# Performance work log

Hardware: AMD Instinct MI355X
Metric: run time of the kernel (lower is better)

The kernel has to match this reference:

```python
import jax, jax.numpy as jnp
from jax import lax
import numpy as np

DN = ('NCHW', 'OIHW', 'NCHW')


def conv(x, w, b, pad=0):
    y = lax.conv_general_dilated(x, w, (1, 1), [(pad, pad), (pad, pad)],
                                 dimension_numbers=DN)
    return y + b[None, :, None, None]


def deconv(x, w, b, stride=1):
    # PyTorch ConvTranspose2d weight is (in, out, kH, kW); equivalent conv uses
    # flipped, in/out-transposed kernel with lhs dilation = stride, pad = k-1.
    k = w.shape[2]
    wt = jnp.flip(w, (2, 3)).transpose(1, 0, 2, 3)
    y = lax.conv_general_dilated(x, wt, (1, 1), [(k - 1, k - 1), (k - 1, k - 1)],
                                 lhs_dilation=(stride, stride), dimension_numbers=DN)
    return y + b[None, :, None, None]


def maxpool2(x):
    return lax.reduce_window(x, -jnp.inf, lax.max, (1, 1, 2, 2), (1, 1, 2, 2), 'VALID')


def setup_inputs() -> dict:
    key = jax.random.key(0)
    ks = jax.random.split(key, 12)
    B = 256

    def he(k, shape, fan_in):
        return jax.random.normal(k, shape, jnp.float32) * np.sqrt(2.0 / fan_in)

    inp = {
        'x': jax.random.normal(ks[0], (B, 1, 28, 28), jnp.float32),
        # encoder convs
        'w1': he(ks[1], (128, 1, 5, 5), 1 * 25), 'b1': jnp.zeros((128,), jnp.float32),
        'w2': he(ks[2], (128, 128, 5, 5), 128 * 25), 'b2': jnp.zeros((128,), jnp.float32),
        'w3': he(ks[3], (128, 128, 5, 5), 128 * 25), 'b3': jnp.zeros((128,), jnp.float32),
        # decoder transposed convs (torch shape: in, out, kH, kW)
        't1w': he(ks[4], (128, 128, 4, 4), 128 * 16), 't1b': jnp.zeros((128,), jnp.float32),
        't2w': he(ks[5], (128, 128, 4, 4), 128 * 16), 't2b': jnp.zeros((128,), jnp.float32),
        't3w': he(ks[6], (128, 128, 5, 5), 128 * 25), 't3b': jnp.zeros((128,), jnp.float32),
        't4w': he(ks[7], (128, 128, 5, 5), 128 * 25), 't4b': jnp.zeros((128,), jnp.float32),
        # mu_net 1x1 conv
        'mw': he(ks[8], (1, 128, 1, 1), 128), 'mb': jnp.zeros((1,), jnp.float32),
        # codebook: Embedding(128, 128), init ~ N(0, 1)
        'dict_w': jax.random.normal(ks[9], (128, 128), jnp.float32),
    }
    return inp


def reference(x, w1, b1, w2, b2, w3, b3,
              t1w, t1b, t2w, t2b, t3w, t3b, t4w, t4b,
              mw, mb, dict_w):
    BETA, RATE = 0.25, 5.0
    # ---- encoder ----
    h = jax.nn.relu(conv(x, w1, b1, pad=0))          # (B,128,24,24)
    h = jax.nn.relu(conv(h, w2, b2, pad=2))          # (B,128,24,24)
    h = maxpool2(h)                                  # (B,128,12,12)
    h = conv(h, w3, b3, pad=2)                       # (B,128,12,12)
    z = maxpool2(h)                                  # (B,128,6,6)

    # ---- nearest_neighbor (faithful: argmax of distance, as in the source) ----
    z_sg = lax.stop_gradient(z)
    z2 = jnp.sum(z_sg * z_sg, axis=1, keepdims=True)          # (B,1,6,6)
    w2n = jnp.sum(dict_w * dict_w, axis=1)                     # (K,)
    cross = jnp.einsum('bchw,kc->bkhw', z_sg, lax.stop_gradient(dict_w))
    d2 = z2 + w2n[None, :, None, None] - 2.0 * cross           # (B,K,6,6)
    index = jnp.argmax(d2, axis=1)                             # (B,6,6) int

    # ---- embedding gather ----
    val = dict_w[index].transpose(0, 3, 1, 2)                  # (B,128,6,6)

    # ---- decoder on detached codes ----
    f = lax.stop_gradient(val)
    f = jax.nn.relu(deconv(f, t1w, t1b, stride=1))             # (B,128,9,9)
    f = jax.nn.relu(deconv(f, t2w, t2b, stride=2))             # (B,128,20,20)
    f = jax.nn.relu(deconv(f, t3w, t3b, stride=1))             # (B,128,24,24)
    f = jax.nn.relu(deconv(f, t4w, t4b, stride=1))             # (B,128,28,28)
    mu = conv(f, mw, mb, pad=0)                                # (B,1,28,28)

    loss_rec = jnp.mean((mu - x) ** 2)
    dict_loss = jnp.mean((val - lax.stop_gradient(z)) ** 2) * RATE
    enc_loss = jnp.mean((z - lax.stop_gradient(val)) ** 2) * BETA * RATE
    var_loss = jnp.zeros((), jnp.float32)
    losses = jnp.stack([loss_rec, dict_loss, enc_loss, var_loss])
    return losses, index
```

## Files before the change

kernel.cpp:

```cpp
#include <hip/hip_runtime.h>
#include <hip/hip_bf16.h>


#define B_ 256

typedef __attribute__((ext_vector_type(8))) short s16x8;
typedef __attribute__((ext_vector_type(4))) short s16x4;
typedef __attribute__((ext_vector_type(8))) _Float16 f16x8;
typedef __attribute__((ext_vector_type(4))) float f32x4;

__device__ inline ushort f2bf(float f) {
  union { __hip_bfloat16 h; ushort u; } cv;
  cv.h = __float2bfloat16(f);
  return cv.u;
}

__global__ __launch_bounds__(256) void prep_all(
    const float* __restrict__ t1w, const float* __restrict__ t3w,
    const float* __restrict__ t4w, const float* __restrict__ t2w,
    const float* __restrict__ w2, const float* __restrict__ w3,
    ushort* __restrict__ wp1, ushort* __restrict__ wp3,
    ushort* __restrict__ wp4, ushort* __restrict__ wp2,
    _Float16* __restrict__ w2h, _Float16* __restrict__ w2l,
    _Float16* __restrict__ w3h, _Float16* __restrict__ w3l) {
  const int b = blockIdx.x, t = threadIdx.x;
  if (b < 1024) {
    int idx = b * 256 + t;
    int ci = idx & 127, co = (idx >> 7) & 127, tap = idx >> 14;
    wp1[idx] = f2bf(t1w[((size_t)ci * 128 + co) * 16 + (15 - tap)]);
  } else if (b < 2624) {
    int idx = (b - 1024) * 256 + t;
    int ci = idx & 127, co = (idx >> 7) & 127, tap = idx >> 14;
    wp3[idx] = f2bf(t3w[((size_t)ci * 128 + co) * 25 + (24 - tap)]);
  } else if (b < 4224) {
    int idx = (b - 2624) * 256 + t;
    int ci = idx & 127, co = (idx >> 7) & 127, tap = idx >> 14;
    wp4[idx] = f2bf(t4w[((size_t)ci * 128 + co) * 25 + (24 - tap)]);
  } else if (b < 5248) {
    int idx = (b - 4224) * 256 + t;
    int ci = idx & 127, co = (idx >> 7) & 127;
    int tap = (idx >> 14) & 3, pp = idx >> 16;
    int u = tap >> 1, v = tap & 1, py = pp >> 1, px = pp & 1;
    wp2[idx] = f2bf(
        t2w[(((size_t)ci * 128 + co) * 4 + (py + 2 * u)) * 4 + (px + 2 * v)]);
  } else if (b < 6848) {
    int idx = (b - 5248) * 256 + t;
    int ci = idx & 127, co = (idx >> 7) & 127, tap = idx >> 14;
    float v = w2[((size_t)co * 128 + ci) * 25 + tap];
    _Float16 h = (_Float16)v;
    w2h[idx] = h;
    w2l[idx] = (_Float16)(v - (float)h);
  } else {
    int idx = (b - 6848) * 256 + t;
    int ci = idx & 127, co = (idx >> 7) & 127, tap = idx >> 14;
    float v = w3[((size_t)co * 128 + ci) * 25 + tap];
    _Float16 h = (_Float16)v;
    w3h[idx] = h;
    w3l[idx] = (_Float16)(v - (float)h);
  }
}

__global__ __launch_bounds__(256) void conv1_kernel(
    const float* __restrict__ x, const float* __restrict__ w,
    const float* __restrict__ b, _Float16* __restrict__ oh,
    _Float16* __restrict__ ol) {
  const int n = blockIdx.x;
  __shared__ float xl[784];
  __shared__ float wl[128 * 25];
  __shared__ float bl[128];
  const int t = threadIdx.x;
  for (int e = t; e < 784; e += 256) xl[e] = x[n * 784 + e];
  for (int e = t; e < 3200; e += 256) wl[e] = w[e];
  if (t < 128) bl[t] = b[t];
  __syncthreads();
  const size_t nb = (size_t)n * 73728;
  for (int idx = t; idx < 73728; idx += 256) {
    int co = idx & 127, p = idx >> 7;
    int y = p / 24, xx = p % 24;
    float acc = bl[co];
    const float* wc = &wl[co * 25];
#pragma unroll
    for (int ky = 0; ky < 5; ky++)
#pragma unroll
      for (int kx = 0; kx < 5; kx++)
        acc += xl[(y + ky) * 28 + xx + kx] * wc[ky * 5 + kx];
    float v = fmaxf(acc, 0.f);
    _Float16 h = (_Float16)v;
    oh[nb + idx] = h;
    ol[nb + idx] = (_Float16)(v - (float)h);
  }
}

template <int IW, int K, int PAD, int TR, bool RELU, bool OUT_F32, int PWX>
__global__ __launch_bounds__(256, 3) void conv_mfma_pool(
    const _Float16* __restrict__ inh, const _Float16* __restrict__ inl,
    const _Float16* __restrict__ wph, const _Float16* __restrict__ wpl,
    const float* __restrict__ bias, _Float16* __restrict__ outh,
    _Float16* __restrict__ outl, float* __restrict__ outf) {
  constexpr int IH = IW, OW = IW, OH = IW;
  constexpr int PW = PWX;
  constexpr int SROWS = TR + K - 1;
  constexpr int S = SROWS * PW;
  constexpr int NPOS = TR * OW;
  constexpr int NCH = NPOS / 16;
  constexpr int SCRP = NPOS + 1;
  constexpr int K2 = K * K;
  constexpr int PITCH = 40;
  constexpr int LIN_ELT = S * PITCH;
  constexpr int LIN_BYTES = 2 * LIN_ELT * 2;
  constexpr int SCR_BYTES = 64 * SCRP * 4;
  constexpr int SMEM_BYTES = LIN_BYTES > SCR_BYTES ? LIN_BYTES : SCR_BYTES;
  static_assert(NPOS % 16 == 0, "");
  static_assert(TR % 2 == 0 && OW % 2 == 0, "");
  static_assert(PW >= OW + K - 1, "");
  __shared__ __align__(16) char smem[SMEM_BYTES];
  _Float16* linh = (_Float16*)smem;
  _Float16* linl = linh + LIN_ELT;
  const int n = blockIdx.x;
  const int r0 = blockIdx.y * TR;
  const int t = threadIdx.x;
  const int wv = t >> 6;
  const int lane = t & 63;
  const int nn = lane & 15;
  const int q = lane >> 4;
  f32x4 acc0[NCH], acc1[NCH];
  int boff[NCH];
#pragma unroll
  for (int c = 0; c < NCH; c++) {
    acc0[c] = f32x4{0.f, 0.f, 0.f, 0.f};
    acc1[c] = f32x4{0.f, 0.f, 0.f, 0.f};
    int p = c * 16 + nn;
    boff[c] = ((p / OW) * PW + (p % OW)) * PITCH + q * 8;
  }
  const int rowA = wv * 16 + nn;
  const int rowB = (wv + 4) * 16 + nn;
  for (int cb = 0; cb < 4; cb++) {
    const int ci0 = cb * 32;
    __syncthreads();
    for (int e = t; e < S * 4; e += 256) {
      int sp = e >> 2, j = e & 3;
      int r = sp / PW, c = sp - r * PW;
      int ir = r0 + r - PAD, ic = c - PAD;
      f16x8 vh = {0, 0, 0, 0, 0, 0, 0, 0};
      f16x8 vl = {0, 0, 0, 0, 0, 0, 0, 0};
      if (ir >= 0 && ir < IH && ic >= 0 && ic < IW) {
        size_t g = ((size_t)n * (IH * IW) + ir * IW + ic) * 128 + ci0 + j * 8;
        vh = *(const f16x8*)&inh[g];
        vl = *(const f16x8*)&inl[g];
      }
      int st = sp * PITCH + j * 8;
      *(f16x8*)&linh[st] = vh;
      *(f16x8*)&linl[st] = vl;
    }
    __syncthreads();
    const size_t gA = (size_t)rowA * 128 + ci0 + q * 8;
    const size_t gB = (size_t)rowB * 128 + ci0 + q * 8;
    f16x8 cah0 = *(const f16x8*)&wph[gA];
    f16x8 cal0 = *(const f16x8*)&wpl[gA];
    f16x8 cah1 = *(const f16x8*)&wph[gB];
    f16x8 cal1 = *(const f16x8*)&wpl[gB];
    for (int tap = 0; tap < K2; tap++) {
      f16x8 nah0 = cah0, nal0 = cal0, nah1 = cah1, nal1 = cal1;
      if (tap + 1 < K2) {
        size_t oA = gA + (size_t)(tap + 1) * 16384;
        size_t oB = gB + (size_t)(tap + 1) * 16384;
        nah0 = *(const f16x8*)&wph[oA];
        nal0 = *(const f16x8*)&wpl[oA];
        nah1 = *(const f16x8*)&wph[oB];
        nal1 = *(const f16x8*)&wpl[oB];
      }
      const int ky = tap / K, kx = tap - ky * K;
      const int tp = (ky * PW + kx) * PITCH;
#pragma unroll
      for (int c = 0; c < NCH; c++) {
        int off = boff[c] + tp;
        f16x8 bh = *(const f16x8*)&linh[off];
        f16x8 bl = *(const f16x8*)&linl[off];
        acc0[c] =
            __builtin_amdgcn_mfma_f32_16x16x32_f16(cah0, bh, acc0[c], 0, 0, 0);
        acc0[c] =
            __builtin_amdgcn_mfma_f32_16x16x32_f16(cah0, bl, acc0[c], 0, 0, 0);
        acc0[c] =
            __builtin_amdgcn_mfma_f32_16x16x32_f16(cal0, bh, acc0[c], 0, 0, 0);
        acc1[c] =
            __builtin_amdgcn_mfma_f32_16x16x32_f16(cah1, bh, acc1[c], 0, 0, 0);
        acc1[c] =
            __builtin_amdgcn_mfma_f32_16x16x32_f16(cah1, bl, acc1[c], 0, 0, 0);
        acc1[c] =
            __builtin_amdgcn_mfma_f32_16x16x32_f16(cal1, bh, acc1[c], 0, 0, 0);
      }
      cah0 = nah0; cal0 = nal0; cah1 = nah1; cal1 = nal1;
    }
  }
  __syncthreads();
  float* scr = (float*)smem + wv * 16 * SCRP;
#pragma unroll
  for (int j = 0; j < 2; j++) {
    const int cot = (j ? wv + 4 : wv) * 16;
#pragma unroll
    for (int c = 0; c < NCH; c++) {
      f32x4 a = j ? acc1[c] : acc0[c];
#pragma unroll
      for (int r = 0; r < 4; r++) {
        float v = a[r] + bias[cot + q * 4 + r];
        if (RELU) v = fmaxf(v, 0.f);
        scr[(q * 4 + r) * SCRP + c * 16 + nn] = v;
      }
    }
    __syncthreads();
    for (int e = lane; e < 16 * (TR / 2) * (OW / 2); e += 64) {
      int co_l = e & 15;
      int rem = e >> 4;
      int pr = rem / (OW / 2), pc = rem - pr * (OW / 2);
      const float* s = scr + co_l * SCRP;
      int lp = (2 * pr) * OW + 2 * pc;
      float m =
          fmaxf(fmaxf(s[lp], s[lp + 1]), fmaxf(s[lp + OW], s[lp + OW + 1]));
      int sp_out = (r0 / 2 + pr) * (OW / 2) + pc;
      size_t go =
          ((size_t)n * ((OH / 2) * (OW / 2)) + sp_out) * 128 + cot + co_l;
      if (OUT_F32) {
        outf[go] = m;
      } else {
        _Float16 h = (_Float16)m;
        outh[go] = h;
        outl[go] = (_Float16)(m - (float)h);
      }
    }
    __syncthreads();
  }
}

__global__ __launch_bounds__(256) void vq_kernel(
    const float* __restrict__ z, const float* __restrict__ dict,
    float* __restrict__ val, ushort* __restrict__ val_bf,
    float* __restrict__ out_idx, float* __restrict__ out) {
  const int n = blockIdx.x;
  __shared__ float zl[36 * 128];
  __shared__ float d2[36 * 129];
  __shared__ float w2n[128];
  __shared__ int bk[36];
  __shared__ float red[256];
  const int t = threadIdx.x;
  const float* zn = z + (size_t)n * 4608;
  for (int e = t; e < 4608; e += 256) zl[e] = zn[e];
  if (t < 128) {
    float s = 0.f;
    const float* wr = dict + t * 128;
    for (int c = 0; c < 128; c++) s += wr[c] * wr[c];
    w2n[t] = s;
  }
  __syncthreads();
  const int k = t & 127, pg = t >> 7;
  float dot[18];
#pragma unroll
  for (int i = 0; i < 18; i++) dot[i] = 0.f;
  const float* wr = dict + k * 128;
  for (int c = 0; c < 128; c++) {
    float wv = wr[c];
#pragma unroll
    for (int i = 0; i < 18; i++) dot[i] += zl[(pg * 18 + i) * 128 + c] * wv;
  }
  float wn = w2n[k];
#pragma unroll
  for (int i = 0; i < 18; i++) d2[(pg * 18 + i) * 129 + k] = wn - 2.f * dot[i];
  __syncthreads();
  if (t < 36) {
    const float* dr = &d2[t * 129];
    float best = dr[0];
    int bi = 0;
    for (int kk = 1; kk < 128; kk++) {
      float v = dr[kk];
      if (v > best) { best = v; bi = kk; }
    }
    bk[t] = bi;
    out_idx[n * 36 + t] = (float)bi;
  }
  __syncthreads();
  float* vn = val + (size_t)n * 4608;
  ushort* vbn = val_bf + (size_t)n * 4608;
  float lsum = 0.f;
  for (int e = t; e < 4608; e += 256) {
    int c = e & 127, p = e >> 7;
    float v = dict[bk[p] * 128 + c];
    vn[e] = v;
    vbn[e] = f2bf(v);
    float d = v - zl[e];
    lsum += d * d;
  }
  red[t] = lsum;
  __syncthreads();
  for (int off = 128; off > 0; off >>= 1) {
    if (t < off) red[t] += red[t + off];
    __syncthreads();
  }
  if (t == 0) {
    atomicAdd(out + 1, red[0] * (5.f / 1179648.f));
    atomicAdd(out + 2, red[0] * (1.25f / 1179648.f));
  }
}

template <int IH, int IW, int OH, int OW, int K, int TR, bool MU_FUSE, int PWX>
__global__ __launch_bounds__(256, 2) void deconv_mfma(
    const ushort* __restrict__ in, const ushort* __restrict__ wprep,
    const float* __restrict__ bias, const float* __restrict__ mw,
    void* __restrict__ outp) {
  constexpr int PAD = K - 1;
  constexpr int PW = PWX;
  constexpr int K2 = K * K;
  constexpr int SROWS = TR + K - 1;
  constexpr int S = SROWS * PW;
  constexpr int NPOS = TR * OW;
  constexpr int NCH = (NPOS + 15) / 16;
  constexpr int PITCH = 40;
  constexpr int LIN_ELT = S * PITCH;
  constexpr int NSTG = (S * 4 + 255) / 256;
  static_assert(PW >= OW + K - 1, "");
  __shared__ __align__(16) ushort lin[2][LIN_ELT];
  const int n = blockIdx.x;
  const int r0 = blockIdx.y * TR;
  const int t = threadIdx.x;
  const int wv = t >> 6;
  const int lane = t & 63;
  const int nn = lane & 15;
  const int q = lane >> 4;
  f32x4 acc0[NCH], acc1[NCH];
  int boff[NCH];
#pragma unroll
  for (int c = 0; c < NCH; c++) {
    acc0[c] = f32x4{0.f, 0.f, 0.f, 0.f};
    acc1[c] = f32x4{0.f, 0.f, 0.f, 0.f};
    int p = c * 16 + nn;
    int pc = p < NPOS ? p : NPOS - 1;
    boff[c] = ((pc / OW) * PW + (pc % OW)) * PITCH + q * 8;
  }
  s16x8 stg[NSTG];
  auto load_stage = [&](int ci0) {
#pragma unroll
    for (int i = 0; i < NSTG; i++) {
      int e = t + i * 256;
      s16x8 v = {0, 0, 0, 0, 0, 0, 0, 0};
      if (e < S * 4) {
        int sp = e >> 2, j = e & 3;
        int rr = sp / PW, cc = sp - rr * PW;
        int ir = r0 + rr - PAD, ic = cc - PAD;
        if (ir >= 0 && ir < IH && ic >= 0 && ic < IW)
          v = *(const s16x8*)&in[((size_t)n * (IH * IW) + ir * IW + ic) * 128 +
                                 ci0 + j * 8];
      }
      stg[i] = v;
    }
  };
  auto store_stage = [&](int bsel) {
#pragma unroll
    for (int i = 0; i < NSTG; i++) {
      int e = t + i * 256;
      if (e < S * 4) {
        int sp = e >> 2, j = e & 3;
        *(s16x8*)&lin[bsel][sp * PITCH + j * 8] = stg[i];
      }
    }
  };

  load_stage(0);
  store_stage(0);
  __syncthreads();
  for (int cb = 0; cb < 4; cb++) {
    const int ci0 = cb * 32;
    if (cb < 3) load_stage(ci0 + 32);
    const ushort* L = lin[cb & 1];
    const size_t gA = (size_t)(wv * 16 + nn) * 128 + ci0 + q * 8;
    const size_t gB = (size_t)((wv + 4) * 16 + nn) * 128 + ci0 + q * 8;
    s16x8 ca0 = *(const s16x8*)&wprep[gA];
    s16x8 ca1 = *(const s16x8*)&wprep[gB];
    for (int tap = 0; tap < K2; tap++) {
      s16x8 na0 = ca0, na1 = ca1;
      if (tap + 1 < K2) {
        na0 = *(const s16x8*)&wprep[gA + (size_t)(tap + 1) * 16384];
        na1 = *(const s16x8*)&wprep[gB + (size_t)(tap + 1) * 16384];
      }
      const int ky = tap / K, kx = tap - ky * K;
      const int tp = (ky * PW + kx) * PITCH;
#pragma unroll
      for (int c = 0; c < NCH; c++) {
        s16x8 b = *(const s16x8*)&L[boff[c] + tp];
        acc0[c] =
            __builtin_amdgcn_mfma_f32_16x16x32_bf16(ca0, b, acc0[c], 0, 0, 0);
        acc1[c] =
            __builtin_amdgcn_mfma_f32_16x16x32_bf16(ca1, b, acc1[c], 0, 0, 0);
      }
      ca0 = na0; ca1 = na1;
    }
    if (cb < 3) {
      store_stage((cb + 1) & 1);
      __syncthreads();
    }
  }
  const int co_a = wv * 16 + q * 4;
  const int co_b = (wv + 4) * 16 + q * 4;
  float ba[4], bb[4];
#pragma unroll
  for (int r = 0; r < 4; r++) {
    ba[r] = bias[co_a + r];
    bb[r] = bias[co_b + r];
  }
  if (!MU_FUSE) {
    ushort* out = (ushort*)outp;
#pragma unroll
    for (int c = 0; c < NCH; c++) {
      int p = c * 16 + nn;
      if (p < NPOS) {
        size_t go = ((size_t)n * (OH * OW) + r0 * OW + p) * 128;
        s16x4 pa, pb;
#pragma unroll
        for (int r = 0; r < 4; r++) {
          pa[r] = (short)f2bf(fmaxf(acc0[c][r] + ba[r], 0.f));
          pb[r] = (short)f2bf(fmaxf(acc1[c][r] + bb[r], 0.f));
        }
        *(s16x4*)&out[go + co_a] = pa;
        *(s16x4*)&out[go + co_b] = pb;
      }
    }
  } else {
    float* out = (float*)outp;
    float wa[4], wb[4];
#pragma unroll
    for (int r = 0; r < 4; r++) {
      wa[r] = mw[co_a + r];
      wb[r] = mw[co_b + r];
    }
#pragma unroll
    for (int c = 0; c < NCH; c++) {
      int p = c * 16 + nn;
      float s = 0.f;
#pragma unroll
      for (int r = 0; r < 4; r++) {
        s += fmaxf(acc0[c][r] + ba[r], 0.f) * wa[r];
        s += fmaxf(acc1[c][r] + bb[r], 0.f) * wb[r];
      }
      s += __shfl_xor(s, 16);
      s += __shfl_xor(s, 32);
      if (q == 0 && p < NPOS)
        atomicAdd(&out[(size_t)n * (OH * OW) + r0 * OW + p], s);
    }
  }
}

__global__ __launch_bounds__(256, 3) void deconv_s2_mfma(
    const ushort* __restrict__ in, const ushort* __restrict__ wp2,
    const float* __restrict__ bias, ushort* __restrict__ out) {
  constexpr int NCH = 7;
  constexpr int PITCH = 40;
  constexpr int PW = 18;
  constexpr int S = 11 * PW;
  const int n = blockIdx.x;
  const int pp = blockIdx.y;
  const int py = pp >> 1, px = pp & 1;
  __shared__ __align__(16) ushort lin[S * PITCH];
  const int t = threadIdx.x;
  const int wv = t >> 6;
  const int lane = t & 63;
  const int nn = lane & 15;
  const int q = lane >> 4;
  f32x4 acc0[NCH], acc1[NCH];
  int boff[NCH];
#pragma unroll
  for (int c = 0; c < NCH; c++) {
    acc0[c] = f32x4{0.f, 0.f, 0.f, 0.f};
    acc1[c] = f32x4{0.f, 0.f, 0.f, 0.f};
    int p = c * 16 + nn;
    int pc = p < 100 ? p : 99;
    boff[c] = ((pc / 10) * PW + (pc % 10)) * PITCH + q * 8;
  }
  const int toffs[4] = {PW + 1, PW, 1, 0};
  for (int cb = 0; cb < 4; cb++) {
    const int ci0 = cb * 32;
    __syncthreads();
    for (int e = t; e < S * 4; e += 256) {
      int sp = e >> 2, j = e & 3;
      int r = sp / PW, c2 = sp - r * PW;
      int ir = r - 1, ic = c2 - 1;
      s16x8 v = {0, 0, 0, 0, 0, 0, 0, 0};
      if (ir >= 0 && ir < 9 && ic >= 0 && ic < 9)
        v = *(const s16x8*)&in[((size_t)n * 81 + ir * 9 + ic) * 128 + ci0 +
                               j * 8];
      *(s16x8*)&lin[sp * PITCH + j * 8] = v;
    }
    __syncthreads();
    const size_t gA =
        ((size_t)(pp * 4) * 128 + wv * 16 + nn) * 128 + ci0 + q * 8;
    const size_t gB =
        ((size_t)(pp * 4) * 128 + (wv + 4) * 16 + nn) * 128 + ci0 + q * 8;
    s16x8 ca0 = *(const s16x8*)&wp2[gA];
    s16x8 ca1 = *(const s16x8*)&wp2[gB];
    for (int tap = 0; tap < 4; tap++) {
      s16x8 na0 = ca0, na1 = ca1;
      if (tap + 1 < 4) {
        na0 = *(const s16x8*)&wp2[gA + (size_t)(tap + 1) * 16384];
        na1 = *(const s16x8*)&wp2[gB + (size_t)(tap + 1) * 16384];
      }
      const int tp = toffs[tap] * PITCH;
#pragma unroll
      for (int c = 0; c < NCH; c++) {
        s16x8 b = *(const s16x8*)&lin[boff[c] + tp];
        acc0[c] =
            __builtin_amdgcn_mfma_f32_16x16x32_bf16(ca0, b, acc0[c], 0, 0, 0);
        acc1[c] =
            __builtin_amdgcn_mfma_f32_16x16x32_bf16(ca1, b, acc1[c], 0, 0, 0);
      }
      ca0 = na0; ca1 = na1;
    }
  }
  const int co_a = wv * 16 + q * 4;
  const int co_b = (wv + 4) * 16 + q * 4;
#pragma unroll
  for (int c = 0; c < NCH; c++) {
    int p = c * 16 + nn;
    if (p < 100) {
      int oy = 2 * (p / 10) + py, ox = 2 * (p % 10) + px;
      size_t go = ((size_t)n * 400 + oy * 20 + ox) * 128;
      s16x4 pa, pb;
#pragma unroll
      for (int r = 0; r < 4; r++) {
        pa[r] = (short)f2bf(fmaxf(acc0[c][r] + bias[co_a + r], 0.f));
        pb[r] = (short)f2bf(fmaxf(acc1[c][r] + bias[co_b + r], 0.f));
      }
      *(s16x4*)&out[go + co_a] = pa;
      *(s16x4*)&out[go + co_b] = pb;
    }
  }
}

__global__ __launch_bounds__(256) void loss_kernel(
    const float4* __restrict__ mu4, const float* __restrict__ mb,
    const float4* __restrict__ x4, float* __restrict__ out) {
  const int b = blockIdx.x, t = threadIdx.x;
  __shared__ float red[256];
  int i = b * 256 + t;
  float4 m = mu4[i], xx = x4[i];
  float b0 = mb[0];
  float d0 = m.x + b0 - xx.x;
  float d1 = m.y + b0 - xx.y;
  float d2 = m.z + b0 - xx.z;
  float d3 = m.w + b0 - xx.w;
  red[t] = d0 * d0 + d1 * d1 + d2 * d2 + d3 * d3;
  __syncthreads();
  for (int off = 128; off > 0; off >>= 1) {
    if (t < off) red[t] += red[t + off];
    __syncthreads();
  }
  if (t == 0) atomicAdd(out, red[0] * (1.0f / 200704.f));
}

extern "C" void kernel_launch(void* const* d_in, const int* in_sizes, int n_in,
                              void* d_out, int out_size, void* d_ws,
                              size_t ws_size, hipStream_t stream) {
  const float* x = (const float*)d_in[0];
  const float* w1 = (const float*)d_in[1];
  const float* b1 = (const float*)d_in[2];
  const float* w2 = (const float*)d_in[3];
  const float* b2 = (const float*)d_in[4];
  const float* w3 = (const float*)d_in[5];
  const float* b3 = (const float*)d_in[6];
  const float* t1w = (const float*)d_in[7];
  const float* t1b = (const float*)d_in[8];
  const float* t2w = (const float*)d_in[9];
  const float* t2b = (const float*)d_in[10];
  const float* t3w = (const float*)d_in[11];
  const float* t3b = (const float*)d_in[12];
  const float* t4w = (const float*)d_in[13];
  const float* t4b = (const float*)d_in[14];
  const float* mw = (const float*)d_in[15];
  const float* mb = (const float*)d_in[16];
  const float* dictw = (const float*)d_in[17];
  float* out = (float*)d_out;

  float* p = (float*)d_ws;
  _Float16* h1h = (_Float16*)p; p += 9437184;
  _Float16* h1l = (_Float16*)p; p += 9437184;
  _Float16* p1h = (_Float16*)p; p += 2359296;
  _Float16* p1l = (_Float16*)p; p += 2359296;
  float* z = p; p += 1179648;
  float* val = p; p += 1179648;
  ushort* val_bf = (ushort*)p; p += 589824;
  float* mu = p; p += 200704;
  ushort* wp1 = (ushort*)p; p += 131072;
  ushort* wp3 = (ushort*)p; p += 204800;
  ushort* wp4 = (ushort*)p; p += 204800;
  ushort* wp2 = (ushort*)p; p += 131072;
  _Float16* w2h = (_Float16*)p; p += 204800;
  _Float16* w2l = (_Float16*)p; p += 204800;
  _Float16* w3h = (_Float16*)p; p += 204800;
  _Float16* w3l = (_Float16*)p; p += 204800;
  ushort* f1 = (ushort*)p1h;
  ushort* f2 = (ushort*)h1l;
  ushort* f3 = (ushort*)h1h;

  hipMemsetAsync(d_out, 0, 4 * sizeof(float), stream);
  hipMemsetAsync(mu, 0, 200704 * sizeof(float), stream);

  prep_all<<<8448, 256, 0, stream>>>(t1w, t3w, t4w, t2w, w2, w3, wp1, wp3, wp4,
                                     wp2, w2h, w2l, w3h, w3l);

  conv1_kernel<<<B_, 256, 0, stream>>>(x, w1, b1, h1h, h1l);
  conv_mfma_pool<24, 5, 2, 6, true, false, 28>
      <<<dim3(B_, 4), 256, 0, stream>>>(h1h, h1l, w2h, w2l, b2, p1h, p1l,
                                        nullptr);
  conv_mfma_pool<12, 5, 2, 4, false, true, 20>
      <<<dim3(B_, 3), 256, 0, stream>>>(p1h, p1l, w3h, w3l, b3, nullptr,
                                        nullptr, z);
  vq_kernel<<<B_, 256, 0, stream>>>(z, dictw, val, val_bf, out + 4, out);
  deconv_mfma<6, 6, 9, 9, 4, 9, false, 17>
      <<<dim3(B_, 1), 256, 0, stream>>>(val_bf, wp1, t1b, nullptr, f1);
  deconv_s2_mfma<<<dim3(B_, 4), 256, 0, stream>>>(f1, wp2, t2b, f2);
  deconv_mfma<20, 20, 24, 24, 5, 8, false, 28>
      <<<dim3(B_, 3), 256, 0, stream>>>(f2, wp3, t3b, nullptr, f3);
  deconv_mfma<24, 24, 28, 28, 5, 7, true, 36>
      <<<dim3(B_, 4), 256, 0, stream>>>(f3, wp4, t4b, mw, mu);
  loss_kernel<<<196, 256, 0, stream>>>((const float4*)mu, mb,
                                       (const float4*)x, out);
}
```

Measured before the change: 881.4 us.

## Fuse conv1 into weight prep kernel and single-buffer deconv LDS staging

Merges the conv1 kernel into the weight-prep kernel as the first 256 blocks, so one launch does both jobs and conv1 can overlap with weight repacking. In deconv_mfma, replaces the double-buffered shared input tile with a single buffer plus an extra barrier before each store. This halves LDS per block, which may allow more resident blocks, but it serializes the stage store behind the compute. The fused kernel now reserves conv1's shared memory for every prep block, which could reduce occupancy for the prep part.

New measurement: 875.6 us, median of 2. No clear change (-0.7%).

```diff
diff --git a/kernel.cpp b/kernel.cpp
--- a/kernel.cpp
+++ b/kernel.cpp
@@ -15,7 +15,10 @@
   return cv.u;
 }
 
-__global__ __launch_bounds__(256) void prep_all(
+__global__ __launch_bounds__(256) void conv1_prep_kernel(
+    const float* __restrict__ x, const float* __restrict__ w1,
+    const float* __restrict__ b1, _Float16* __restrict__ oh,
+    _Float16* __restrict__ ol,
     const float* __restrict__ t1w, const float* __restrict__ t3w,
     const float* __restrict__ t4w, const float* __restrict__ t2w,
     const float* __restrict__ w2, const float* __restrict__ w3,
@@ -23,7 +26,35 @@
     ushort* __restrict__ wp4, ushort* __restrict__ wp2,
     _Float16* __restrict__ w2h, _Float16* __restrict__ w2l,
     _Float16* __restrict__ w3h, _Float16* __restrict__ w3l) {
-  const int b = blockIdx.x, t = threadIdx.x;
+  const int t = threadIdx.x;
+  if (blockIdx.x < 256) {
+    const int n = blockIdx.x;
+    __shared__ float xl[784];
+    __shared__ float wl[128 * 25];
+    __shared__ float bl[128];
+    for (int e = t; e < 784; e += 256) xl[e] = x[n * 784 + e];
+    for (int e = t; e < 3200; e += 256) wl[e] = w1[e];
+    if (t < 128) bl[t] = b1[t];
+    __syncthreads();
+    const size_t nb = (size_t)n * 73728;
+    for (int idx = t; idx < 73728; idx += 256) {
+      int co = idx & 127, p = idx >> 7;
+      int y = p / 24, xx = p % 24;
+      float acc = bl[co];
+      const float* wc = &wl[co * 25];
+#pragma unroll
+      for (int ky = 0; ky < 5; ky++)
+#pragma unroll
+        for (int kx = 0; kx < 5; kx++)
+          acc += xl[(y + ky) * 28 + xx + kx] * wc[ky * 5 + kx];
+      float v = fmaxf(acc, 0.f);
+      _Float16 h = (_Float16)v;
+      oh[nb + idx] = h;
+      ol[nb + idx] = (_Float16)(v - (float)h);
+    }
+    return;
+  }
+  const int b = blockIdx.x - 256;
   if (b < 1024) {
     int idx = b * 256 + t;
     int ci = idx & 127, co = (idx >> 7) & 127, tap = idx >> 14;
@@ -57,37 +88,6 @@
     _Float16 h = (_Float16)v;
     w3h[idx] = h;
     w3l[idx] = (_Float16)(v - (float)h);
-  }
-}
-
-__global__ __launch_bounds__(256) void conv1_kernel(
-    const float* __restrict__ x, const float* __restrict__ w,
-    const float* __restrict__ b, _Float16* __restrict__ oh,
-    _Float16* __restrict__ ol) {
-  const int n = blockIdx.x;
-  __shared__ float xl[784];
-  __shared__ float wl[128 * 25];
-  __shared__ float bl[128];
-  const int t = threadIdx.x;
-  for (int e = t; e < 784; e += 256) xl[e] = x[n * 784 + e];
-  for (int e = t; e < 3200; e += 256) wl[e] = w[e];
-  if (t < 128) bl[t] = b[t];
-  __syncthreads();
-  const size_t nb = (size_t)n * 73728;
-  for (int idx = t; idx < 73728; idx += 256) {
-    int co = idx & 127, p = idx >> 7;
-    int y = p / 24, xx = p % 24;
-    float acc = bl[co];
-    const float* wc = &wl[co * 25];
-#pragma unroll
-    for (int ky = 0; ky < 5; ky++)
-#pragma unroll
-      for (int kx = 0; kx < 5; kx++)
-        acc += xl[(y + ky) * 28 + xx + kx] * wc[ky * 5 + kx];
-    float v = fmaxf(acc, 0.f);
-    _Float16 h = (_Float16)v;
-    oh[nb + idx] = h;
-    ol[nb + idx] = (_Float16)(v - (float)h);
   }
 }
 
@@ -316,7 +316,7 @@
   constexpr int LIN_ELT = S * PITCH;
   constexpr int NSTG = (S * 4 + 255) / 256;
   static_assert(PW >= OW + K - 1, "");
-  __shared__ __align__(16) ushort lin[2][LIN_ELT];
+  __shared__ __align__(16) ushort lin[LIN_ELT];
   const int n = blockIdx.x;
   const int r0 = blockIdx.y * TR;
   const int t = threadIdx.x;
@@ -351,24 +351,23 @@
       stg[i] = v;
     }
   };
-  auto store_stage = [&](int bsel) {
+  auto store_stage = [&]() {
 #pragma unroll
     for (int i = 0; i < NSTG; i++) {
       int e = t + i * 256;
       if (e < S * 4) {
         int sp = e >> 2, j = e & 3;
-        *(s16x8*)&lin[bsel][sp * PITCH + j * 8] = stg[i];
+        *(s16x8*)&lin[sp * PITCH + j * 8] = stg[i];
       }
     }
   };
 
   load_stage(0);
-  store_stage(0);
+  store_stage();
   __syncthreads();
   for (int cb = 0; cb < 4; cb++) {
     const int ci0 = cb * 32;
     if (cb < 3) load_stage(ci0 + 32);
-    const ushort* L = lin[cb & 1];
     const size_t gA = (size_t)(wv * 16 + nn) * 128 + ci0 + q * 8;
     const size_t gB = (size_t)((wv + 4) * 16 + nn) * 128 + ci0 + q * 8;
     s16x8 ca0 = *(const s16x8*)&wprep[gA];
@@ -383,7 +382,7 @@
       const int tp = (ky * PW + kx) * PITCH;
 #pragma unroll
       for (int c = 0; c < NCH; c++) {
-        s16x8 b = *(const s16x8*)&L[boff[c] + tp];
+        s16x8 b = *(const s16x8*)&lin[boff[c] + tp];
         acc0[c] =
             __builtin_amdgcn_mfma_f32_16x16x32_bf16(ca0, b, acc0[c], 0, 0, 0);
         acc1[c] =
@@ -392,7 +391,8 @@
       ca0 = na0; ca1 = na1;
     }
     if (cb < 3) {
-      store_stage((cb + 1) & 1);
+      __syncthreads();
+      store_stage();
       __syncthreads();
     }
   }
@@ -599,10 +599,9 @@
   hipMemsetAsync(d_out, 0, 4 * sizeof(float), stream);
   hipMemsetAsync(mu, 0, 200704 * sizeof(float), stream);
 
-  prep_all<<<8448, 256, 0, stream>>>(t1w, t3w, t4w, t2w, w2, w3, wp1, wp3, wp4,
-                                     wp2, w2h, w2l, w3h, w3l);
-
-  conv1_kernel<<<B_, 256, 0, stream>>>(x, w1, b1, h1h, h1l);
+  conv1_prep_kernel<<<8704, 256, 0, stream>>>(
+      x, w1, b1, h1h, h1l, t1w, t3w, t4w, t2w, w2, w3, wp1, wp3, wp4, wp2,
+      w2h, w2l, w3h, w3l);
   conv_mfma_pool<24, 5, 2, 6, true, false, 28>
       <<<dim3(B_, 4), 256, 0, stream>>>(h1h, h1l, w2h, w2l, b2, p1h, p1l,
                                         nullptr);
```
